# Performance work log

Hardware: AMD Instinct MI355X
Metric: run time of the kernel (lower is better)

## Reference

```python
import jax, jax.numpy as jnp
import numpy as np
import math

N_PATCH = 216   # 6^3 sliding patches of a 20^3 tensor
DIM = 125       # 5^3 flattened patch
HEADS = 8
HEAD_DIM = 64
NSIDE = 6
EPS_BN = 1e-5
EPS_NORM = 1e-12


def batchnorm_train(x, w, b):
    # x: [B, C, H, W]; training-mode BN: biased batch stats over (B, H, W)
    mean = jnp.mean(x, axis=(0, 2, 3), keepdims=True)
    var = jnp.mean((x - mean) ** 2, axis=(0, 2, 3), keepdims=True)
    xh = (x - mean) / jnp.sqrt(var + EPS_BN)
    return xh * w[None, :, None, None] + b[None, :, None, None]


def l2_normalize(x, axis):
    n = jnp.sqrt(jnp.sum(x * x, axis=axis, keepdims=True))
    return x / jnp.maximum(n, EPS_NORM)


def sparsemax_dim1(z):
    # z: [B, N, M]; sparsemax along axis=1
    n = z.shape[1]
    zs = -jnp.sort(-z, axis=1)                       # descending sort
    ks = jnp.arange(1, n + 1, dtype=z.dtype)[None, :, None]
    cs = jnp.cumsum(zs, axis=1)
    support = 1.0 + ks * zs > cs                     # support set indicator
    k_star = jnp.sum(support, axis=1, keepdims=True).astype(z.dtype)
    tau = (jnp.sum(jnp.where(support, zs, 0.0), axis=1, keepdims=True) - 1.0) / k_star
    return jnp.maximum(z - tau, 0.0)


def setup_inputs() -> dict:
    key = jax.random.key(0)
    ks = jax.random.split(key, 6)
    return {
        "patches": jax.random.normal(ks[0], (1, N_PATCH, 5, 5, 5), jnp.float32),
        "Wq": jax.random.normal(ks[1], (HEADS * HEAD_DIM, DIM), jnp.float32) * 0.05,
        "Wk": jax.random.normal(ks[2], (HEADS * HEAD_DIM, DIM), jnp.float32) * 0.05,
        "bn_weight": jnp.ones((HEADS,), jnp.float32),
        "bn_bias": jnp.zeros((HEADS,), jnp.float32),
        "W1": jax.random.normal(ks[3], (20, 72), jnp.float32) * 0.05,
        "W2": jax.random.normal(ks[4], (20, 72), jnp.float32) * 0.05,
        "W3": jax.random.normal(ks[5], (20, 72), jnp.float32) * 0.05,
    }


def reference(patches, Wq, Wk, bn_weight, bn_bias, W1, W2, W3):
    B = 1
    x = patches.reshape(B, N_PATCH, DIM)                       # [1,216,125]
    q = x @ Wq.T                                               # [1,216,512]
    k = x @ Wk.T
    Q = q.reshape(B, N_PATCH, HEADS, HEAD_DIM).transpose(0, 2, 1, 3)  # [1,8,216,64]
    K = k.reshape(B, N_PATCH, HEADS, HEAD_DIM).transpose(0, 2, 1, 3)
    Q = l2_normalize(batchnorm_train(Q, bn_weight, bn_bias), axis=3)
    K = l2_normalize(batchnorm_train(K, bn_weight, bn_bias), axis=3)
    scores = jnp.einsum('bhnd,bhmd->bhnm', Q, K) / math.sqrt(DIM)     # [1,8,216,216]
    scores = scores.transpose(0, 2, 1, 3).reshape(B, N_PATCH, HEADS * N_PATCH)
    att = sparsemax_dim1(scores)                               # [1,216,1728] (dropout=eval)
    # [2,2,2,6,6,6,6,6,6] -> permute -> [1,72,72,72]
    x4 = att.reshape(2, 2, 2, NSIDE, NSIDE, NSIDE, NSIDE, NSIDE, NSIDE)
    x4 = x4.transpose(0, 3, 6, 1, 4, 7, 2, 5, 8).reshape(1, 72, 72, 72)
    # TCL: multi-mode contraction with factors [20,72]
    x5 = jnp.einsum('bijk,ai,cj,dk->bacd', x4, W1, W2, W3)     # [1,20,20,20]
    return jnp.tanh(x5), att
```

## Files before the change

### kernel.cpp

```cpp
#include <hip/hip_runtime.h>
#include <hip/hip_bf16.h>
#include <float.h>

#define N_PATCH 216
#define DIM 125
#define HEADS 8
#define HEAD_DIM 64
#define QK 512
#define NH (HEADS*N_PATCH)


__global__ __launch_bounds__(256) void k_wt(const float* __restrict__ Wq,
        const float* __restrict__ Wk, float* __restrict__ Wt, float* __restrict__ stats) {
    __shared__ float lds[64*DIM];
    const int bid = blockIdx.x;
    const int t = threadIdx.x;
    if (bid == 0 && t < 32) stats[t] = 0.f;
    const float* src = (bid < 8) ? Wq : Wk;
    const int rbase = (bid & 7)*64*DIM;
    for (int idx = t; idx < 64*DIM; idx += 256)
        lds[idx] = src[rbase + idx];
    __syncthreads();
    const int lane = t & 63, ii = t >> 6;
    const int c0 = bid*64;
    for (int i = ii; i < DIM; i += 4)
        Wt[i*1024 + c0 + lane] = lds[lane*DIM + i];
}

__global__ __launch_bounds__(512) void k_qk(const float* __restrict__ x,
        const float* __restrict__ Wt, float* __restrict__ q, float* __restrict__ k,
        float* __restrict__ stats) {
    __shared__ float xs[DIM];
    const int n = blockIdx.x, t = threadIdx.x;
    if (t < DIM) xs[t] = x[n*DIM + t];
    __syncthreads();
    const float2* Wt2 = (const float2*)Wt;
    float2 acc = {0.f, 0.f};
    #pragma unroll 5
    for (int i = 0; i < DIM; ++i) {
        float2 w = Wt2[i*512 + t];
        float xv = xs[i];
        acc.x = fmaf(xv, w.x, acc.x);
        acc.y = fmaf(xv, w.y, acc.y);
    }
    int c = 2*t;
    if (c < QK) *(float2*)(q + n*QK + c) = acc;
    else        *(float2*)(k + n*QK + (c - QK)) = acc;
    float s  = acc.x + acc.y;
    float ss = acc.x*acc.x + acc.y*acc.y;
    #pragma unroll
    for (int off = 16; off; off >>= 1) {
        s  += __shfl_down(s,  off, 32);
        ss += __shfl_down(ss, off, 32);
    }
    if ((t & 31) == 0) {
        int isK = (c >= QK) ? 1 : 0;
        int h = (c & (QK-1)) >> 6;
        atomicAdd(&stats[(isK*8+h)*2],   s);
        atomicAdd(&stats[(isK*8+h)*2+1], ss);
    }
}

__global__ __launch_bounds__(256) void k_norm(const float* __restrict__ q,
        const float* __restrict__ k, const float* __restrict__ stats,
        const float* __restrict__ bnw, const float* __restrict__ bnb,
        float* __restrict__ Qt, float* __restrict__ Kn) {
    int gw = blockIdx.x*4 + (threadIdx.x >> 6);
    int lane = threadIdx.x & 63;
    int isK = (gw >= NH) ? 1 : 0;
    int r = isK ? gw - NH : gw;
    int h = r / N_PATCH, n = r % N_PATCH;
    const float* src = isK ? k : q;
    int sb = (isK*8 + h)*2;
    const float invN = 1.0f/13824.0f;
    float mean = stats[sb]*invN;
    float var  = stats[sb+1]*invN - mean*mean;
    float inv = 1.0f / sqrtf(var + 1e-5f);
    float w = bnw[h], b = bnb[h];
    float v = src[n*QK + h*HEAD_DIM + lane];
    float xh = (v - mean)*inv*w + b;
    float sq = xh*xh;
    #pragma unroll
    for (int off = 32; off; off >>= 1) sq += __shfl_xor(sq, off, 64);
    float nrm = fmaxf(sqrtf(sq), 1e-12f);
    float o = xh / nrm;
    if (isK) Kn[(h*N_PATCH + n)*HEAD_DIM + lane] = o;
    else     Qt[h*HEAD_DIM*N_PATCH + lane*N_PATCH + n] = o;
}

__global__ __launch_bounds__(256) void k_sparse(const float* __restrict__ Qt,
        const float* __restrict__ Kn, float* __restrict__ att, float* __restrict__ x4) {
    const int wv = threadIdx.x >> 6, lane = threadIdx.x & 63;
    const int c = blockIdx.x*4 + wv;
    const int h = c / N_PATCH, m = c % N_PATCH;
    __shared__ float ks[4][HEAD_DIM];
    ks[wv][lane] = Kn[(h*N_PATCH+m)*HEAD_DIM + lane];
    __syncthreads();
    const float* qh = Qt + h*HEAD_DIM*N_PATCH;
    float z0=0.f, z1=0.f, z2=0.f, z3=0.f;
    const bool v3 = (lane < N_PATCH - 192);
    #pragma unroll 8
    for (int d = 0; d < HEAD_DIM; ++d) {
        float kd = ks[wv][d];
        z0 = fmaf(qh[d*N_PATCH + lane],       kd, z0);
        z1 = fmaf(qh[d*N_PATCH + 64 + lane],  kd, z1);
        z2 = fmaf(qh[d*N_PATCH + 128 + lane], kd, z2);
        if (v3) z3 = fmaf(qh[d*N_PATCH + 192 + lane], kd, z3);
    }
    const float scale = 0.08944271909999159f;
    z0 *= scale; z1 *= scale; z2 *= scale; z3 *= scale;
    float mx = fmaxf(fmaxf(z0, z1), fmaxf(z2, v3 ? z3 : -FLT_MAX));
    #pragma unroll
    for (int off = 32; off; off >>= 1) mx = fmaxf(mx, __shfl_xor(mx, off, 64));
    float tau = mx - 1.0f;
    for (int it = 0; it < 48; ++it) {
        float g = fmaxf(z0-tau,0.f) + fmaxf(z1-tau,0.f) + fmaxf(z2-tau,0.f)
                + (v3 ? fmaxf(z3-tau,0.f) : 0.f);
        float cnt = (z0>tau ? 1.f:0.f) + (z1>tau ? 1.f:0.f) + (z2>tau ? 1.f:0.f)
                  + ((v3 && z3>tau) ? 1.f:0.f);
        #pragma unroll
        for (int off = 32; off; off >>= 1) {
            g   += __shfl_xor(g,   off, 64);
            cnt += __shfl_xor(cnt, off, 64);
        }
        g -= 1.0f;
        if (g <= 1e-7f) break;
        tau += g / cnt;
    }
    #pragma unroll
    for (int j = 0; j < 4; ++j) {
        int n = lane + 64*j;
        if (n >= N_PATCH) break;
        float zz = (j==0) ? z0 : (j==1) ? z1 : (j==2) ? z2 : z3;
        float a = fmaxf(zz - tau, 0.f);
        att[n*NH + c] = a;
        int nh2 = n / 27;
        int d0 = nh2 >> 2, d1 = (nh2 >> 1) & 1, d2 = nh2 & 1;
        int r = (n % 27)*NH + c;
        int d3 = r / 7776; r -= d3*7776;
        int d4 = r / 1296; r -= d4*1296;
        int d5 = r / 216;  r -= d5*216;
        int d6 = r / 36;   r -= d6*36;
        int d7 = r / 6;
        int d8 = r - d7*6;
        int ii  = d0*36 + d3*6 + d6;
        int jj  = d1*36 + d4*6 + d7;
        int kk2 = d2*36 + d5*6 + d8;
        x4[(ii*72 + jj)*72 + kk2] = a;
    }
}

__global__ __launch_bounds__(256) void k_tcl1(const float* __restrict__ W1,
        const float* __restrict__ x4, float* __restrict__ t1) {
    int o = blockIdx.x*256 + threadIdx.x;
    int a = o / 5184, jk = o % 5184;
    float acc = 0.f;
    #pragma unroll 8
    for (int i = 0; i < 72; ++i) acc += W1[a*72+i]*x4[i*5184 + jk];
    t1[o] = acc;
}

__global__ __launch_bounds__(512) void k_tcl23(const float* __restrict__ W2,
        const float* __restrict__ W3, const float* __restrict__ t1,
        float* __restrict__ out0) {
    __shared__ float t1a[5184];
    __shared__ float t2a[1440];
    const int a = blockIdx.x, t = threadIdx.x;
    for (int i = t; i < 5184; i += 512) t1a[i] = t1[a*5184 + i];
    __syncthreads();
    for (int idx = t; idx < 1440; idx += 512) {
        int cc = idx / 72, kk = idx % 72;
        float acc = 0.f;
        #pragma unroll 8
        for (int j = 0; j < 72; ++j) acc += W2[cc*72+j]*t1a[j*72 + kk];
        t2a[idx] = acc;
    }
    __syncthreads();
    if (t < 400) {
        int cc = t / 20, dd = t % 20;
        float acc = 0.f;
        #pragma unroll 8
        for (int kq = 0; kq < 72; ++kq) acc += W3[dd*72+kq]*t2a[cc*72 + kq];
        out0[(a*20 + cc)*20 + dd] = tanhf(acc);
    }
}

extern "C" void kernel_launch(void* const* d_in, const int* in_sizes, int n_in,
                              void* d_out, int out_size, void* d_ws, size_t ws_size,
                              hipStream_t stream) {
    const float* patches = (const float*)d_in[0];
    const float* Wq = (const float*)d_in[1];
    const float* Wk = (const float*)d_in[2];
    const float* bnw = (const float*)d_in[3];
    const float* bnb = (const float*)d_in[4];
    const float* W1 = (const float*)d_in[5];
    const float* W2 = (const float*)d_in[6];
    const float* W3 = (const float*)d_in[7];
    float* out = (float*)d_out;
    float* ws = (float*)d_ws;

    float* Wt    = ws;
    float* q     = ws + 128000;
    float* k     = ws + 238592;
    float* stats = ws + 349184;
    float* Qt    = ws + 349216;
    float* Kn    = ws + 459808;
    float* x4    = ws + 570400;
    float* t1    = ws + 943648;

    float* out0 = out;
    float* att  = out + 8000;

    hipLaunchKernelGGL(k_wt,     dim3(16),   dim3(256), 0, stream, Wq, Wk, Wt, stats);
    hipLaunchKernelGGL(k_qk,     dim3(216),  dim3(512), 0, stream, patches, Wt, q, k, stats);
    hipLaunchKernelGGL(k_norm,   dim3(864),  dim3(256), 0, stream, q, k, stats, bnw, bnb, Qt, Kn);
    hipLaunchKernelGGL(k_sparse, dim3(432),  dim3(256), 0, stream, Qt, Kn, att, x4);
    hipLaunchKernelGGL(k_tcl1,   dim3(405),  dim3(256), 0, stream, W1, x4, t1);
    hipLaunchKernelGGL(k_tcl23,  dim3(20),   dim3(512), 0, stream, W2, W3, t1, out0);
}
```

Baseline: 162.0 us.

## Fuse weight transpose into QK projection and cap sparsemax Newton iterations

Replaces the separate weight-transpose kernel and per-patch projection kernel with one kernel. Each of its 32 blocks stages a 32-column slice of Wq or Wk in LDS and loops over all patches, eight at a time. The stats buffer is now zeroed with a memset, and BN statistics are reduced per block before the atomic adds. The sparsemax threshold iteration is capped at 20 steps with a looser tolerance (1e-6 instead of 1e-7), which risks a slightly less exact tau. The fused kernel uses only 32 blocks, so parallelism is much lower, and it loops 27 passes with two barriers each.

```diff
diff --git a/kernel.cpp b/kernel.cpp
--- a/kernel.cpp
+++ b/kernel.cpp
@@ -10,54 +10,47 @@
 #define NH (HEADS*N_PATCH)
 
 
-__global__ __launch_bounds__(256) void k_wt(const float* __restrict__ Wq,
-        const float* __restrict__ Wk, float* __restrict__ Wt, float* __restrict__ stats) {
-    __shared__ float lds[64*DIM];
-    const int bid = blockIdx.x;
-    const int t = threadIdx.x;
-    if (bid == 0 && t < 32) stats[t] = 0.f;
-    const float* src = (bid < 8) ? Wq : Wk;
-    const int rbase = (bid & 7)*64*DIM;
-    for (int idx = t; idx < 64*DIM; idx += 256)
-        lds[idx] = src[rbase + idx];
-    __syncthreads();
-    const int lane = t & 63, ii = t >> 6;
-    const int c0 = bid*64;
-    for (int i = ii; i < DIM; i += 4)
-        Wt[i*1024 + c0 + lane] = lds[lane*DIM + i];
-}
-
-__global__ __launch_bounds__(512) void k_qk(const float* __restrict__ x,
-        const float* __restrict__ Wt, float* __restrict__ q, float* __restrict__ k,
-        float* __restrict__ stats) {
-    __shared__ float xs[DIM];
-    const int n = blockIdx.x, t = threadIdx.x;
-    if (t < DIM) xs[t] = x[n*DIM + t];
-    __syncthreads();
-    const float2* Wt2 = (const float2*)Wt;
-    float2 acc = {0.f, 0.f};
-    #pragma unroll 5
-    for (int i = 0; i < DIM; ++i) {
-        float2 w = Wt2[i*512 + t];
-        float xv = xs[i];
-        acc.x = fmaf(xv, w.x, acc.x);
-        acc.y = fmaf(xv, w.y, acc.y);
-    }
-    int c = 2*t;
-    if (c < QK) *(float2*)(q + n*QK + c) = acc;
-    else        *(float2*)(k + n*QK + (c - QK)) = acc;
-    float s  = acc.x + acc.y;
-    float ss = acc.x*acc.x + acc.y*acc.y;
-    #pragma unroll
-    for (int off = 16; off; off >>= 1) {
-        s  += __shfl_down(s,  off, 32);
-        ss += __shfl_down(ss, off, 32);
-    }
-    if ((t & 31) == 0) {
-        int isK = (c >= QK) ? 1 : 0;
-        int h = (c & (QK-1)) >> 6;
-        atomicAdd(&stats[(isK*8+h)*2],   s);
-        atomicAdd(&stats[(isK*8+h)*2+1], ss);
+__global__ __launch_bounds__(256) void k_qkw(const float* __restrict__ x,
+        const float* __restrict__ Wq, const float* __restrict__ Wk,
+        float* __restrict__ q, float* __restrict__ k, float* __restrict__ stats) {
+    __shared__ float Wl[32*DIM];
+    __shared__ float xsb[8][DIM];
+    __shared__ float rs[4], rss[4];
+    const int b = blockIdx.x, t = threadIdx.x;
+    const int isK = b >> 4;
+    const int c0 = (b & 15) * 32;
+    const float* Wsrc = isK ? Wk : Wq;
+    for (int idx = t; idx < 32*DIM; idx += 256)
+        Wl[idx] = Wsrc[c0*DIM + idx];
+    const int col = t & 31, nsub = t >> 5;
+    float* dst = isK ? k : q;
+    float s = 0.f, ss = 0.f;
+    for (int pass = 0; pass < 27; ++pass) {
+        __syncthreads();
+        for (int idx = t; idx < 8*DIM; idx += 256)
+            xsb[idx/DIM][idx%DIM] = x[(pass*8 + idx/DIM)*DIM + idx%DIM];
+        __syncthreads();
+        float acc = 0.f;
+        #pragma unroll 5
+        for (int i = 0; i < DIM; ++i)
+            acc = fmaf(xsb[nsub][i], Wl[col*DIM + i], acc);
+        dst[(pass*8 + nsub)*QK + c0 + col] = acc;
+        s += acc; ss += acc*acc;
+    }
+    #pragma unroll
+    for (int off = 32; off; off >>= 1) {
+        s  += __shfl_down(s,  off, 64);
+        ss += __shfl_down(ss, off, 64);
+    }
+    const int wv = t >> 6, lane = t & 63;
+    if (lane == 0) { rs[wv] = s; rss[wv] = ss; }
+    __syncthreads();
+    if (t == 0) {
+        float S  = rs[0]+rs[1]+rs[2]+rs[3];
+        float SS = rss[0]+rss[1]+rss[2]+rss[3];
+        int h = (b & 15) >> 1;
+        atomicAdd(&stats[(isK*8+h)*2],   S);
+        atomicAdd(&stats[(isK*8+h)*2+1], SS);
     }
 }
 
@@ -113,7 +106,7 @@
     #pragma unroll
     for (int off = 32; off; off >>= 1) mx = fmaxf(mx, __shfl_xor(mx, off, 64));
     float tau = mx - 1.0f;
-    for (int it = 0; it < 48; ++it) {
+    for (int it = 0; it < 20; ++it) {
         float g = fmaxf(z0-tau,0.f) + fmaxf(z1-tau,0.f) + fmaxf(z2-tau,0.f)
                 + (v3 ? fmaxf(z3-tau,0.f) : 0.f);
         float cnt = (z0>tau ? 1.f:0.f) + (z1>tau ? 1.f:0.f) + (z2>tau ? 1.f:0.f)
@@ -124,7 +117,7 @@
             cnt += __shfl_xor(cnt, off, 64);
         }
         g -= 1.0f;
-        if (g <= 1e-7f) break;
+        if (g <= 1e-6f) break;
         tau += g / cnt;
     }
     #pragma unroll
@@ -199,7 +192,6 @@
     float* out = (float*)d_out;
     float* ws = (float*)d_ws;
 
-    float* Wt    = ws;
     float* q     = ws + 128000;
     float* k     = ws + 238592;
     float* stats = ws + 349184;
@@ -211,10 +203,10 @@
     float* out0 = out;
     float* att  = out + 8000;
 
-    hipLaunchKernelGGL(k_wt,     dim3(16),   dim3(256), 0, stream, Wq, Wk, Wt, stats);
-    hipLaunchKernelGGL(k_qk,     dim3(216),  dim3(512), 0, stream, patches, Wt, q, k, stats);
-    hipLaunchKernelGGL(k_norm,   dim3(864),  dim3(256), 0, stream, q, k, stats, bnw, bnb, Qt, Kn);
-    hipLaunchKernelGGL(k_sparse, dim3(432),  dim3(256), 0, stream, Qt, Kn, att, x4);
-    hipLaunchKernelGGL(k_tcl1,   dim3(405),  dim3(256), 0, stream, W1, x4, t1);
-    hipLaunchKernelGGL(k_tcl23,  dim3(20),   dim3(512), 0, stream, W2, W3, t1, out0);
-}
+    hipMemsetAsync(stats, 0, 32*sizeof(float), stream);
+    hipLaunchKernelGGL(k_qkw,   dim3(32),   dim3(256), 0, stream, patches, Wq, Wk, q, k, stats);
+    hipLaunchKernelGGL(k_norm,  dim3(864),  dim3(256), 0, stream, q, k, stats, bnw, bnb, Qt, Kn);
+    hipLaunchKernelGGL(k_sparse,dim3(432),  dim3(256), 0, stream, Qt, Kn, att, x4);
+    hipLaunchKernelGGL(k_tcl1,  dim3(405),  dim3(256), 0, stream, W1, x4, t1);
+    hipLaunchKernelGGL(k_tcl23, dim3(20),   dim3(512), 0, stream, W2, W3, t1, out0);
+}
```

After: 195.3 us. 20.5% more time.
